# Kernel tuning notes

Measured on AMD Instinct MI355X. Metric: run time of the kernel, lower is better.

## Reference

```python
import jax, jax.numpy as jnp
import numpy as np

B_SZ, SEQ, D_IN, D_ST, D_OUT = 16, 8192, 128, 128, 128


def setup_inputs() -> dict:
    key = jax.random.key(0)
    ku, ka, kb, kc, kd = jax.random.split(key, 5)
    u = jax.random.normal(ku, (B_SZ, SEQ, D_IN), dtype=jnp.float32)
    # A scaled to spectral radius ~0.9 so the long recurrence stays stable
    A = jax.random.normal(ka, (D_ST, D_ST), dtype=jnp.float32) * (0.9 / np.sqrt(D_ST))
    B = jax.random.normal(kb, (D_ST, D_IN), dtype=jnp.float32) * (1.0 / np.sqrt(D_IN))
    C = jax.random.normal(kc, (D_OUT, D_ST), dtype=jnp.float32) * (1.0 / np.sqrt(D_ST))
    D = jax.random.normal(kd, (D_OUT, D_IN), dtype=jnp.float32) * (1.0 / np.sqrt(D_IN))
    return {"u": u, "A": A, "B": B, "C": C, "D": D}


def reference(u, A, B, C, D):
    # x_t = x_{t-1} A^T + u_t B^T ; y_t = x_t C^T + u_t D^T ; x_0 = 0
    batch = u.shape[0]
    state0 = jnp.zeros((batch, A.shape[0]), dtype=u.dtype)

    def step(state, u_t):  # state: [B, S_dim], u_t: [B, D_in]
        new_state = state @ A.T + u_t @ B.T
        y = new_state @ C.T + u_t @ D.T
        return new_state, y

    u_t_first = jnp.swapaxes(u, 0, 1)  # [SEQ, B, D_in]
    _, ys = jax.lax.scan(step, state0, u_t_first)
    return jnp.swapaxes(ys, 0, 1)  # [B, SEQ, D_out]
```

## Files before the change

kernel.cpp:

```cpp
#include <hip/hip_runtime.h>


#define SEQ 8192
#define BS  16
#define DD  128
#define CL  32
#define NC  256
#define GRP 16
#define NG  16

typedef __bf16 bf16t;
typedef __bf16 bf16x8 __attribute__((ext_vector_type(8)));
typedef __bf16 bf16x4 __attribute__((ext_vector_type(4)));
typedef float  f32x4  __attribute__((ext_vector_type(4)));

#define MFMA(a,b,c) __builtin_amdgcn_mfma_f32_16x16x32_bf16(a,b,c,0,0,0)

__device__ __forceinline__ int swz(int b, int j) { return j ^ ((b & 7) << 3); }

struct Frag { bf16x8 h[4]; bf16x8 l[4]; };

__device__ __forceinline__ void load_frag_T(const float* __restrict__ src, int lane, int w, Frag& f) {
    int n  = (w << 4) + (lane & 15);
    int kb = ((lane >> 4) & 3) << 3;
#pragma unroll
    for (int q = 0; q < 4; q++) {
        const float* p = src + n * DD + (q << 5) + kb;
#pragma unroll
        for (int e = 0; e < 8; e++) {
            float v = p[e];
            bf16t hh = (bf16t)v;
            f.h[q][e] = hh;
            f.l[q][e] = (bf16t)(v - (float)hh);
        }
    }
}

__device__ __forceinline__ void load_frag_N(const float* __restrict__ src, int lane, int w, Frag& f) {
    int n  = (w << 4) + (lane & 15);
    int kb = ((lane >> 4) & 3) << 3;
#pragma unroll
    for (int q = 0; q < 4; q++) {
#pragma unroll
        for (int e = 0; e < 8; e++) {
            float v = src[((q << 5) + kb + e) * DD + n];
            bf16t hh = (bf16t)v;
            f.h[q][e] = hh;
            f.l[q][e] = (bf16t)(v - (float)hh);
        }
    }
}

__device__ __forceinline__ bf16x8 afrag(const bf16t* __restrict__ X, int lane, int q) {
    int b  = lane & 15;
    int j0 = (q << 5) + (((lane >> 4) & 3) << 3);
    return *(const bf16x8*)(X + b * DD + swz(b, j0));
}

__device__ __forceinline__ void put_state(bf16t* __restrict__ H, bf16t* __restrict__ L,
                                          int lane, int w, f32x4 acc) {
    int n = (w << 4) + (lane & 15);
#pragma unroll
    for (int r = 0; r < 4; r++) {
        int b = (((lane >> 4) & 3) << 2) + r;
        float v = acc[r];
        bf16t hh = (bf16t)v;
        H[b * DD + swz(b, n)] = hh;
        L[b * DD + swz(b, n)] = (bf16t)(v - (float)hh);
    }
}

__device__ __forceinline__ void stage_rows(const float* __restrict__ src, long rs,
                                           bf16t* __restrict__ H, bf16t* __restrict__ L, int tid) {
    int b  = tid >> 5;
    int j0 = (tid & 31) << 2;
    float4 v = *(const float4*)(src + (long)b * rs + j0);
    float vv[4] = { v.x, v.y, v.z, v.w };
    bf16x4 h, l;
#pragma unroll
    for (int e = 0; e < 4; e++) {
        bf16t hh = (bf16t)vv[e];
        h[e] = hh;
        l[e] = (bf16t)(vv[e] - (float)hh);
    }
    *(bf16x4*)(H + b * DD + swz(b, j0)) = h;
    *(bf16x4*)(L + b * DD + swz(b, j0)) = l;
}

__device__ __forceinline__ f32x4 load_accfrag(const float* __restrict__ src, int lane, int w) {
    int n = (w << 4) + (lane & 15);
    f32x4 a;
#pragma unroll
    for (int r = 0; r < 4; r++) {
        int b = (((lane >> 4) & 3) << 2) + r;
        a[r] = src[b * DD + n];
    }
    return a;
}

__device__ __forceinline__ void store_accfrag(float* __restrict__ dst, int lane, int w,
                                              f32x4 a, long rs) {
    int n = (w << 4) + (lane & 15);
#pragma unroll
    for (int r = 0; r < 4; r++) {
        int b = (((lane >> 4) & 3) << 2) + r;
        dst[(long)b * rs + n] = a[r];
    }
}

__global__ __launch_bounds__(512) void k_chunk(const float* __restrict__ u,
                                               const float* __restrict__ A,
                                               const float* __restrict__ B,
                                               float* __restrict__ E,
                                               float* __restrict__ P) {
    __shared__ __align__(16) bf16t Xh[2][BS * DD], Xl[2][BS * DD];
    __shared__ __align__(16) bf16t Uh[2][BS * DD], Ul[2][BS * DD];
    int tid = threadIdx.x, lane = tid & 63, w = tid >> 6;
    bool ident = blockIdx.x >= NC;
    int g2 = blockIdx.x - NC;

    Frag fA, fB;
    load_frag_T(A, lane, w, fA);
    if (!ident) load_frag_T(B, lane, w, fB);

    for (int i = tid; i < BS * DD; i += 512) {
        int b = i >> 7, j = swz(b, i & 127);
        float v = (ident && j == g2 * 16 + b) ? 1.f : 0.f;
        Xh[0][i] = (bf16t)v;
        Xl[0][i] = (bf16t)0.f;
    }
    int c = blockIdx.x;
    const float* ubase = u + (long)c * CL * DD;
    int b_ = tid >> 5, j0_ = (tid & 31) << 2;
    if (!ident) stage_rows(ubase, (long)SEQ * DD, Uh[0], Ul[0], tid);
    __syncthreads();

    int p = 0;
    f32x4 acc = {0.f, 0.f, 0.f, 0.f};
    for (int i = 0; i < CL; i++) {
        float4 un = {0.f, 0.f, 0.f, 0.f};
        if (!ident && i + 1 < CL)
            un = *(const float4*)(ubase + (long)b_ * SEQ * DD + (i + 1) * DD + j0_);
        f32x4 ax = {0.f,0.f,0.f,0.f}, ax2 = {0.f,0.f,0.f,0.f};
#pragma unroll
        for (int q = 0; q < 4; q++) {
            bf16x8 xh = afrag(Xh[p], lane, q), xl = afrag(Xl[p], lane, q);
            ax  = MFMA(xh, fA.h[q], ax);
            ax2 = MFMA(xl, fA.h[q], ax2);
            ax  = MFMA(xh, fA.l[q], ax);
            if (!ident) {
                bf16x8 uh = afrag(Uh[i & 1], lane, q), ul = afrag(Ul[i & 1], lane, q);
                ax2 = MFMA(uh, fB.h[q], ax2);
                ax  = MFMA(ul, fB.h[q], ax);
                ax2 = MFMA(uh, fB.l[q], ax2);
            }
        }
        acc = ax + ax2;
        if (i + 1 < CL) {
            put_state(Xh[p ^ 1], Xl[p ^ 1], lane, w, acc);
            if (!ident) {
                float vv[4] = { un.x, un.y, un.z, un.w };
                bf16x4 h, l;
#pragma unroll
                for (int e = 0; e < 4; e++) {
                    bf16t hh = (bf16t)vv[e];
                    h[e] = hh;
                    l[e] = (bf16t)(vv[e] - (float)hh);
                }
                *(bf16x4*)(Uh[(i + 1) & 1] + b_ * DD + swz(b_, j0_)) = h;
                *(bf16x4*)(Ul[(i + 1) & 1] + b_ * DD + swz(b_, j0_)) = l;
            }
            __syncthreads();
            p ^= 1;
        }
    }
    if (!ident) store_accfrag(E + (long)c * BS * DD, lane, w, acc, DD);
    else        store_accfrag(P + (long)g2 * 16 * DD, lane, w, acc, DD);
}

__global__ __launch_bounds__(512) void k_group(const float* __restrict__ E,
                                               const float* __restrict__ P,
                                               float* __restrict__ E2,
                                               float* __restrict__ Pg) {
    __shared__ __align__(16) bf16t Xh[2][BS * DD], Xl[2][BS * DD];
    int tid = threadIdx.x, lane = tid & 63, w = tid >> 6;
    bool ident = blockIdx.x >= NG;
    int g2 = blockIdx.x - NG;
    Frag fP;
    load_frag_N(P, lane, w, fP);
    for (int i = tid; i < BS * DD; i += 512) {
        int b = i >> 7, j = swz(b, i & 127);
        float v = (ident && j == g2 * 16 + b) ? 1.f : 0.f;
        Xh[0][i] = (bf16t)v;
        Xl[0][i] = (bf16t)0.f;
    }
    __syncthreads();
    int p = 0, g = blockIdx.x;
    f32x4 acc = {0.f, 0.f, 0.f, 0.f};
    for (int r = 0; r < GRP; r++) {
        f32x4 a1 = {0.f,0.f,0.f,0.f}, a2 = {0.f,0.f,0.f,0.f};
        if (!ident) a1 = load_accfrag(E + (long)(g * GRP + r) * BS * DD, lane, w);
#pragma unroll
        for (int q = 0; q < 4; q++) {
            bf16x8 xh = afrag(Xh[p], lane, q), xl = afrag(Xl[p], lane, q);
            a1 = MFMA(xh, fP.h[q], a1);
            a2 = MFMA(xl, fP.h[q], a2);
            a1 = MFMA(xh, fP.l[q], a1);
        }
        acc = a1 + a2;
        if (r + 1 < GRP) {
            put_state(Xh[p ^ 1], Xl[p ^ 1], lane, w, acc);
            __syncthreads();
            p ^= 1;
        }
    }
    if (!ident) store_accfrag(E2 + (long)g * BS * DD, lane, w, acc, DD);
    else        store_accfrag(Pg + (long)g2 * 16 * DD, lane, w, acc, DD);
}

__global__ __launch_bounds__(512) void k_top(const float* __restrict__ E2,
                                             const float* __restrict__ Pg,
                                             float* __restrict__ S2) {
    __shared__ __align__(16) bf16t Xh[2][BS * DD], Xl[2][BS * DD];
    int tid = threadIdx.x, lane = tid & 63, w = tid >> 6;
    Frag fP;
    load_frag_N(Pg, lane, w, fP);
    for (int i = tid; i < BS * DD; i += 512) {
        Xh[0][i] = (bf16t)0.f;
        Xl[0][i] = (bf16t)0.f;
    }
    __syncthreads();
    int p = 0;
    f32x4 T = {0.f, 0.f, 0.f, 0.f};
    for (int g = 0; g < NG; g++) {
        store_accfrag(S2 + (long)g * BS * DD, lane, w, T, DD);
        f32x4 a1 = load_accfrag(E2 + (long)g * BS * DD, lane, w), a2 = {0.f,0.f,0.f,0.f};
#pragma unroll
        for (int q = 0; q < 4; q++) {
            bf16x8 xh = afrag(Xh[p], lane, q), xl = afrag(Xl[p], lane, q);
            a1 = MFMA(xh, fP.h[q], a1);
            a2 = MFMA(xl, fP.h[q], a2);
            a1 = MFMA(xh, fP.l[q], a1);
        }
        T = a1 + a2;
        if (g + 1 < NG) {
            put_state(Xh[p ^ 1], Xl[p ^ 1], lane, w, T);
            __syncthreads();
            p ^= 1;
        }
    }
}

__global__ __launch_bounds__(512) void k_fix(const float* __restrict__ E,
                                             const float* __restrict__ P,
                                             const float* __restrict__ S2,
                                             float* __restrict__ S) {
    __shared__ __align__(16) bf16t Xh[2][BS * DD], Xl[2][BS * DD];
    int tid = threadIdx.x, lane = tid & 63, w = tid >> 6;
    int g = blockIdx.x;
    Frag fP;
    load_frag_N(P, lane, w, fP);
    stage_rows(S2 + (long)g * BS * DD, DD, Xh[0], Xl[0], tid);
    f32x4 T = load_accfrag(S2 + (long)g * BS * DD, lane, w);
    __syncthreads();
    int p = 0;
    for (int r = 0; r < GRP; r++) {
        int c = g * GRP + r;
        store_accfrag(S + (long)c * BS * DD, lane, w, T, DD);
        if (r + 1 == GRP) break;
        f32x4 a1 = load_accfrag(E + (long)c * BS * DD, lane, w), a2 = {0.f,0.f,0.f,0.f};
#pragma unroll
        for (int q = 0; q < 4; q++) {
            bf16x8 xh = afrag(Xh[p], lane, q), xl = afrag(Xl[p], lane, q);
            a1 = MFMA(xh, fP.h[q], a1);
            a2 = MFMA(xl, fP.h[q], a2);
            a1 = MFMA(xh, fP.l[q], a1);
        }
        T = a1 + a2;
        put_state(Xh[p ^ 1], Xl[p ^ 1], lane, w, T);
        __syncthreads();
        p ^= 1;
    }
}

__global__ __launch_bounds__(512) void k_main(const float* __restrict__ u,
                                              const float* __restrict__ A,
                                              const float* __restrict__ B,
                                              const float* __restrict__ C,
                                              const float* __restrict__ D,
                                              const float* __restrict__ S,
                                              float* __restrict__ out) {
    __shared__ __align__(16) bf16t Xh[2][BS * DD], Xl[2][BS * DD];
    __shared__ __align__(16) bf16t Uh[2][BS * DD], Ul[2][BS * DD];
    int tid = threadIdx.x, lane = tid & 63, w = tid >> 6;
    Frag fA, fB, fC, fD;
    load_frag_T(A, lane, w, fA);
    load_frag_T(B, lane, w, fB);
    load_frag_T(C, lane, w, fC);
    load_frag_T(D, lane, w, fD);
    int c = blockIdx.x;
    const float* ubase = u + (long)c * CL * DD;
    int b_ = tid >> 5, j0_ = (tid & 31) << 2;
    stage_rows(S + (long)c * BS * DD, DD, Xh[0], Xl[0], tid);
    stage_rows(ubase, (long)SEQ * DD, Uh[0], Ul[0], tid);
    __syncthreads();
    int p = 0;
    for (int i = 0; i < CL; i++) {
        float4 un = {0.f, 0.f, 0.f, 0.f};
        if (i + 1 < CL)
            un = *(const float4*)(ubase + (long)b_ * SEQ * DD + (i + 1) * DD + j0_);
        f32x4 ax = {0.f,0.f,0.f,0.f}, ax2 = {0.f,0.f,0.f,0.f};
        f32x4 ay = {0.f,0.f,0.f,0.f}, ay2 = {0.f,0.f,0.f,0.f};
#pragma unroll
        for (int q = 0; q < 4; q++) {
            bf16x8 xh = afrag(Xh[p], lane, q), xl = afrag(Xl[p], lane, q);
            bf16x8 uh = afrag(Uh[i & 1], lane, q), ul = afrag(Ul[i & 1], lane, q);
            ax  = MFMA(xh, fA.h[q], ax);
            ax2 = MFMA(xl, fA.h[q], ax2);
            ax  = MFMA(xh, fA.l[q], ax);
            ax2 = MFMA(uh, fB.h[q], ax2);
            ax  = MFMA(ul, fB.h[q], ax);
            ax2 = MFMA(uh, fB.l[q], ax2);
            ay  = MFMA(uh, fD.h[q], ay);
            ay2 = MFMA(ul, fD.h[q], ay2);
            ay  = MFMA(uh, fD.l[q], ay);
        }
        f32x4 xnew = ax + ax2;
        put_state(Xh[p ^ 1], Xl[p ^ 1], lane, w, xnew);
        if (i + 1 < CL) {
            float vv[4] = { un.x, un.y, un.z, un.w };
            bf16x4 h, l;
#pragma unroll
            for (int e = 0; e < 4; e++) {
                bf16t hh = (bf16t)vv[e];
                h[e] = hh;
                l[e] = (bf16t)(vv[e] - (float)hh);
            }
            *(bf16x4*)(Uh[(i + 1) & 1] + b_ * DD + swz(b_, j0_)) = h;
            *(bf16x4*)(Ul[(i + 1) & 1] + b_ * DD + swz(b_, j0_)) = l;
        }
        __syncthreads();
#pragma unroll
        for (int q = 0; q < 4; q++) {
            bf16x8 nh = afrag(Xh[p ^ 1], lane, q), nl = afrag(Xl[p ^ 1], lane, q);
            ay  = MFMA(nh, fC.h[q], ay);
            ay2 = MFMA(nl, fC.h[q], ay2);
            ay  = MFMA(nh, fC.l[q], ay);
        }
        f32x4 y = ay + ay2;
        store_accfrag(out + ((long)c * CL + i) * DD, lane, w, y, (long)SEQ * DD);
        p ^= 1;
    }
}

extern "C" void kernel_launch(void* const* d_in, const int* in_sizes, int n_in,
                              void* d_out, int out_size, void* d_ws, size_t ws_size,
                              hipStream_t stream) {
    (void)in_sizes; (void)n_in; (void)out_size; (void)ws_size;
    const float* u = (const float*)d_in[0];
    const float* A = (const float*)d_in[1];
    const float* B = (const float*)d_in[2];
    const float* C = (const float*)d_in[3];
    const float* D = (const float*)d_in[4];
    float* out = (float*)d_out;
    float* ws  = (float*)d_ws;
    float* P  = ws;
    float* Pg = ws + 16384;
    float* E  = ws + 32768;
    float* E2 = ws + 32768 + 524288;
    float* S2 = E2 + 32768;
    float* S  = S2 + 32768;
    dim3 blk(512);
    k_chunk<<<NC + 8, blk, 0, stream>>>(u, A, B, E, P);
    k_group<<<NG + 8, blk, 0, stream>>>(E, P, E2, Pg);
    k_top  <<<1,      blk, 0, stream>>>(E2, Pg, S2);
    k_fix  <<<NG,     blk, 0, stream>>>(E, P, S2, S);
    k_main <<<NC,     blk, 0, stream>>>(u, A, B, C, D, S, out);
}
```

Baseline: 131.7 us.

## Advance recurrence two steps per iteration using precomputed A², AB, CA, CAA products

Precomputes A², AB, CA, CA+D-style combined matrices in two small prep kernels, then advances the state two timesteps per iteration in both the chunk and main kernels. This halves the number of serial dependency steps and barriers per chunk. Outputs are computed directly from the previous state and inputs, so the second C-multiply after the barrier goes away. Output matrices use only the high bf16 part (no split-precision correction), which risks lower accuracy. It also adds two prep launches and more register pressure, with launch bounds hinting two blocks per CU.

```diff
diff --git a/kernel.cpp b/kernel.cpp
--- a/kernel.cpp
+++ b/kernel.cpp
@@ -5,6 +5,7 @@
 #define BS  16
 #define DD  128
 #define CL  32
+#define PH  16
 #define NC  256
 #define GRP 16
 #define NG  16
@@ -18,7 +19,8 @@
 
 __device__ __forceinline__ int swz(int b, int j) { return j ^ ((b & 7) << 3); }
 
-struct Frag { bf16x8 h[4]; bf16x8 l[4]; };
+struct Frag  { bf16x8 h[4]; bf16x8 l[4]; };
+struct FragH { bf16x8 h[4]; };
 
 __device__ __forceinline__ void load_frag_T(const float* __restrict__ src, int lane, int w, Frag& f) {
     int n  = (w << 4) + (lane & 15);
@@ -33,6 +35,17 @@
             f.h[q][e] = hh;
             f.l[q][e] = (bf16t)(v - (float)hh);
         }
+    }
+}
+
+__device__ __forceinline__ void load_frag_T_h(const float* __restrict__ src, int lane, int w, FragH& f) {
+    int n  = (w << 4) + (lane & 15);
+    int kb = ((lane >> 4) & 3) << 3;
+#pragma unroll
+    for (int q = 0; q < 4; q++) {
+        const float* p = src + n * DD + (q << 5) + kb;
+#pragma unroll
+        for (int e = 0; e < 8; e++) f.h[q][e] = (bf16t)p[e];
     }
 }
 
@@ -87,6 +100,20 @@
     *(bf16x4*)(L + b * DD + swz(b, j0)) = l;
 }
 
+__device__ __forceinline__ void write_u(bf16t* __restrict__ H, bf16t* __restrict__ L,
+                                        int b_, int j0_, float4 v) {
+    float vv[4] = { v.x, v.y, v.z, v.w };
+    bf16x4 h, l;
+#pragma unroll
+    for (int e = 0; e < 4; e++) {
+        bf16t hh = (bf16t)vv[e];
+        h[e] = hh;
+        l[e] = (bf16t)(vv[e] - (float)hh);
+    }
+    *(bf16x4*)(H + b_ * DD + swz(b_, j0_)) = h;
+    *(bf16x4*)(L + b_ * DD + swz(b_, j0_)) = l;
+}
+
 __device__ __forceinline__ f32x4 load_accfrag(const float* __restrict__ src, int lane, int w) {
     int n = (w << 4) + (lane & 15);
     f32x4 a;
@@ -108,20 +135,51 @@
     }
 }
 
-__global__ __launch_bounds__(512) void k_chunk(const float* __restrict__ u,
-                                               const float* __restrict__ A,
+__global__ __launch_bounds__(128) void k_prep1(const float* __restrict__ A,
                                                const float* __restrict__ B,
-                                               float* __restrict__ E,
-                                               float* __restrict__ P) {
+                                               const float* __restrict__ C,
+                                               const float* __restrict__ D,
+                                               float* __restrict__ A2m, float* __restrict__ ABm,
+                                               float* __restrict__ Gm,  float* __restrict__ Hm) {
+    int sel = blockIdx.x >> 7, r = blockIdx.x & 127, j = threadIdx.x;
+    const float* L = (sel < 2) ? A : C;
+    const float* R = (sel == 0 || sel == 2) ? A : B;
+    float s = 0.f;
+#pragma unroll 8
+    for (int m = 0; m < 128; m++) s = fmaf(L[r * 128 + m], R[m * 128 + j], s);
+    if      (sel == 0) A2m[r * 128 + j] = s;
+    else if (sel == 1) ABm[r * 128 + j] = s;
+    else if (sel == 2) Gm[r * 128 + j]  = s;
+    else               Hm[r * 128 + j]  = s + D[r * 128 + j];
+}
+
+__global__ __launch_bounds__(128) void k_prep2(const float* __restrict__ A,
+                                               const float* __restrict__ B,
+                                               const float* __restrict__ Gm,
+                                               float* __restrict__ G2m, float* __restrict__ H2m) {
+    int sel = blockIdx.x >> 7, r = blockIdx.x & 127, j = threadIdx.x;
+    const float* R = sel ? B : A;
+    float s = 0.f;
+#pragma unroll 8
+    for (int m = 0; m < 128; m++) s = fmaf(Gm[r * 128 + m], R[m * 128 + j], s);
+    (sel ? H2m : G2m)[r * 128 + j] = s;
+}
+
+__global__ __launch_bounds__(512, 2) void k_chunk(const float* __restrict__ u,
+                                                  const float* __restrict__ A2m,
+                                                  const float* __restrict__ ABm,
+                                                  const float* __restrict__ Bm,
+                                                  float* __restrict__ E,
+                                                  float* __restrict__ P) {
     __shared__ __align__(16) bf16t Xh[2][BS * DD], Xl[2][BS * DD];
-    __shared__ __align__(16) bf16t Uh[2][BS * DD], Ul[2][BS * DD];
+    __shared__ __align__(16) bf16t Uh[2][2][BS * DD], Ul[2][2][BS * DD];
     int tid = threadIdx.x, lane = tid & 63, w = tid >> 6;
     bool ident = blockIdx.x >= NC;
     int g2 = blockIdx.x - NC;
 
-    Frag fA, fB;
-    load_frag_T(A, lane, w, fA);
-    if (!ident) load_frag_T(B, lane, w, fB);
+    Frag fA2, fAB, fB;
+    load_frag_T(A2m, lane, w, fA2);
+    if (!ident) { load_frag_T(ABm, lane, w, fAB); load_frag_T(Bm, lane, w, fB); }
 
     for (int i = tid; i < BS * DD; i += 512) {
         int b = i >> 7, j = swz(b, i & 127);
@@ -132,43 +190,46 @@
     int c = blockIdx.x;
     const float* ubase = u + (long)c * CL * DD;
     int b_ = tid >> 5, j0_ = (tid & 31) << 2;
-    if (!ident) stage_rows(ubase, (long)SEQ * DD, Uh[0], Ul[0], tid);
+    if (!ident) {
+        stage_rows(ubase,      (long)SEQ * DD, Uh[0][0], Ul[0][0], tid);
+        stage_rows(ubase + DD, (long)SEQ * DD, Uh[0][1], Ul[0][1], tid);
+    }
     __syncthreads();
 
     int p = 0;
     f32x4 acc = {0.f, 0.f, 0.f, 0.f};
-    for (int i = 0; i < CL; i++) {
-        float4 un = {0.f, 0.f, 0.f, 0.f};
-        if (!ident && i + 1 < CL)
-            un = *(const float4*)(ubase + (long)b_ * SEQ * DD + (i + 1) * DD + j0_);
-        f32x4 ax = {0.f,0.f,0.f,0.f}, ax2 = {0.f,0.f,0.f,0.f};
+    for (int j = 0; j < PH; j++) {
+        int jb = j & 1;
+        float4 un1 = {0,0,0,0}, un2 = {0,0,0,0};
+        if (!ident && j + 1 < PH) {
+            const float* nb = ubase + (long)b_ * SEQ * DD + (2 * j + 2) * DD + j0_;
+            un1 = *(const float4*)(nb);
+            un2 = *(const float4*)(nb + DD);
+        }
+        f32x4 ax = {0,0,0,0}, ax2 = {0,0,0,0}, ax3 = {0,0,0,0};
 #pragma unroll
         for (int q = 0; q < 4; q++) {
             bf16x8 xh = afrag(Xh[p], lane, q), xl = afrag(Xl[p], lane, q);
-            ax  = MFMA(xh, fA.h[q], ax);
-            ax2 = MFMA(xl, fA.h[q], ax2);
-            ax  = MFMA(xh, fA.l[q], ax);
+            ax  = MFMA(xh, fA2.h[q], ax);
+            ax2 = MFMA(xl, fA2.h[q], ax2);
+            ax3 = MFMA(xh, fA2.l[q], ax3);
             if (!ident) {
-                bf16x8 uh = afrag(Uh[i & 1], lane, q), ul = afrag(Ul[i & 1], lane, q);
-                ax2 = MFMA(uh, fB.h[q], ax2);
-                ax  = MFMA(ul, fB.h[q], ax);
-                ax2 = MFMA(uh, fB.l[q], ax2);
+                bf16x8 u1h = afrag(Uh[jb][0], lane, q), u1l = afrag(Ul[jb][0], lane, q);
+                bf16x8 u2h = afrag(Uh[jb][1], lane, q), u2l = afrag(Ul[jb][1], lane, q);
+                ax  = MFMA(u1h, fAB.h[q], ax);
+                ax2 = MFMA(u1l, fAB.h[q], ax2);
+                ax3 = MFMA(u1h, fAB.l[q], ax3);
+                ax  = MFMA(u2h, fB.h[q], ax);
+                ax2 = MFMA(u2l, fB.h[q], ax2);
+                ax3 = MFMA(u2h, fB.l[q], ax3);
             }
         }
-        acc = ax + ax2;
-        if (i + 1 < CL) {
+        acc = ax + ax2 + ax3;
+        if (j + 1 < PH) {
             put_state(Xh[p ^ 1], Xl[p ^ 1], lane, w, acc);
             if (!ident) {
-                float vv[4] = { un.x, un.y, un.z, un.w };
-                bf16x4 h, l;
-#pragma unroll
-                for (int e = 0; e < 4; e++) {
-                    bf16t hh = (bf16t)vv[e];
-                    h[e] = hh;
-                    l[e] = (bf16t)(vv[e] - (float)hh);
-                }
-                *(bf16x4*)(Uh[(i + 1) & 1] + b_ * DD + swz(b_, j0_)) = h;
-                *(bf16x4*)(Ul[(i + 1) & 1] + b_ * DD + swz(b_, j0_)) = l;
+                write_u(Uh[jb ^ 1][0], Ul[jb ^ 1][0], b_, j0_, un1);
+                write_u(Uh[jb ^ 1][1], Ul[jb ^ 1][1], b_, j0_, un2);
             }
             __syncthreads();
             p ^= 1;
@@ -283,73 +344,82 @@
     }
 }
 
-__global__ __launch_bounds__(512) void k_main(const float* __restrict__ u,
-                                              const float* __restrict__ A,
-                                              const float* __restrict__ B,
-                                              const float* __restrict__ C,
-                                              const float* __restrict__ D,
-                                              const float* __restrict__ S,
-                                              float* __restrict__ out) {
+__global__ __launch_bounds__(512, 2) void k_main(const float* __restrict__ u,
+                                                 const float* __restrict__ A2m,
+                                                 const float* __restrict__ ABm,
+                                                 const float* __restrict__ Bm,
+                                                 const float* __restrict__ Gm,
+                                                 const float* __restrict__ Hm,
+                                                 const float* __restrict__ G2m,
+                                                 const float* __restrict__ H2m,
+                                                 const float* __restrict__ S,
+                                                 float* __restrict__ out) {
     __shared__ __align__(16) bf16t Xh[2][BS * DD], Xl[2][BS * DD];
-    __shared__ __align__(16) bf16t Uh[2][BS * DD], Ul[2][BS * DD];
+    __shared__ __align__(16) bf16t Uh[2][2][BS * DD], Ul[2][2][BS * DD];
     int tid = threadIdx.x, lane = tid & 63, w = tid >> 6;
-    Frag fA, fB, fC, fD;
-    load_frag_T(A, lane, w, fA);
-    load_frag_T(B, lane, w, fB);
-    load_frag_T(C, lane, w, fC);
-    load_frag_T(D, lane, w, fD);
+    Frag fA2, fAB, fB;
+    FragH fG, fH, fG2, fH2;
+    load_frag_T(A2m, lane, w, fA2);
+    load_frag_T(ABm, lane, w, fAB);
+    load_frag_T(Bm,  lane, w, fB);
+    load_frag_T_h(Gm,  lane, w, fG);
+    load_frag_T_h(Hm,  lane, w, fH);
+    load_frag_T_h(G2m, lane, w, fG2);
+    load_frag_T_h(H2m, lane, w, fH2);
     int c = blockIdx.x;
     const float* ubase = u + (long)c * CL * DD;
     int b_ = tid >> 5, j0_ = (tid & 31) << 2;
     stage_rows(S + (long)c * BS * DD, DD, Xh[0], Xl[0], tid);
-    stage_rows(ubase, (long)SEQ * DD, Uh[0], Ul[0], tid);
+    stage_rows(ubase,      (long)SEQ * DD, Uh[0][0], Ul[0][0], tid);
+    stage_rows(ubase + DD, (long)SEQ * DD, Uh[0][1], Ul[0][1], tid);
     __syncthreads();
     int p = 0;
-    for (int i = 0; i < CL; i++) {
-        float4 un = {0.f, 0.f, 0.f, 0.f};
-        if (i + 1 < CL)
-            un = *(const float4*)(ubase + (long)b_ * SEQ * DD + (i + 1) * DD + j0_);
-        f32x4 ax = {0.f,0.f,0.f,0.f}, ax2 = {0.f,0.f,0.f,0.f};
-        f32x4 ay = {0.f,0.f,0.f,0.f}, ay2 = {0.f,0.f,0.f,0.f};
+    for (int j = 0; j < PH; j++) {
+        int jb = j & 1;
+        float4 un1 = {0,0,0,0}, un2 = {0,0,0,0};
+        if (j + 1 < PH) {
+            const float* nb = ubase + (long)b_ * SEQ * DD + (2 * j + 2) * DD + j0_;
+            un1 = *(const float4*)(nb);
+            un2 = *(const float4*)(nb + DD);
+        }
+        f32x4 ax = {0,0,0,0}, ax2 = {0,0,0,0}, ax3 = {0,0,0,0};
+        f32x4 ay1 = {0,0,0,0}, ay1b = {0,0,0,0};
+        f32x4 ay2 = {0,0,0,0}, ay2b = {0,0,0,0}, ay2c = {0,0,0,0};
 #pragma unroll
         for (int q = 0; q < 4; q++) {
-            bf16x8 xh = afrag(Xh[p], lane, q), xl = afrag(Xl[p], lane, q);
-            bf16x8 uh = afrag(Uh[i & 1], lane, q), ul = afrag(Ul[i & 1], lane, q);
-            ax  = MFMA(xh, fA.h[q], ax);
-            ax2 = MFMA(xl, fA.h[q], ax2);
-            ax  = MFMA(xh, fA.l[q], ax);
-            ax2 = MFMA(uh, fB.h[q], ax2);
-            ax  = MFMA(ul, fB.h[q], ax);
-            ax2 = MFMA(uh, fB.l[q], ax2);
-            ay  = MFMA(uh, fD.h[q], ay);
-            ay2 = MFMA(ul, fD.h[q], ay2);
-            ay  = MFMA(uh, fD.l[q], ay);
-        }
-        f32x4 xnew = ax + ax2;
-        put_state(Xh[p ^ 1], Xl[p ^ 1], lane, w, xnew);
-        if (i + 1 < CL) {
-            float vv[4] = { un.x, un.y, un.z, un.w };
-            bf16x4 h, l;
-#pragma unroll
-            for (int e = 0; e < 4; e++) {
-                bf16t hh = (bf16t)vv[e];
-                h[e] = hh;
-                l[e] = (bf16t)(vv[e] - (float)hh);
-            }
-            *(bf16x4*)(Uh[(i + 1) & 1] + b_ * DD + swz(b_, j0_)) = h;
-            *(bf16x4*)(Ul[(i + 1) & 1] + b_ * DD + swz(b_, j0_)) = l;
-        }
-        __syncthreads();
-#pragma unroll
-        for (int q = 0; q < 4; q++) {
-            bf16x8 nh = afrag(Xh[p ^ 1], lane, q), nl = afrag(Xl[p ^ 1], lane, q);
-            ay  = MFMA(nh, fC.h[q], ay);
-            ay2 = MFMA(nl, fC.h[q], ay2);
-            ay  = MFMA(nh, fC.l[q], ay);
-        }
-        f32x4 y = ay + ay2;
-        store_accfrag(out + ((long)c * CL + i) * DD, lane, w, y, (long)SEQ * DD);
-        p ^= 1;
+            bf16x8 xh  = afrag(Xh[p], lane, q),      xl  = afrag(Xl[p], lane, q);
+            bf16x8 u1h = afrag(Uh[jb][0], lane, q),  u1l = afrag(Ul[jb][0], lane, q);
+            bf16x8 u2h = afrag(Uh[jb][1], lane, q),  u2l = afrag(Ul[jb][1], lane, q);
+            ax  = MFMA(xh,  fA2.h[q], ax);
+            ax2 = MFMA(xl,  fA2.h[q], ax2);
+            ax3 = MFMA(xh,  fA2.l[q], ax3);
+            ax  = MFMA(u1h, fAB.h[q], ax);
+            ax2 = MFMA(u1l, fAB.h[q], ax2);
+            ax3 = MFMA(u1h, fAB.l[q], ax3);
+            ax  = MFMA(u2h, fB.h[q],  ax);
+            ax2 = MFMA(u2l, fB.h[q],  ax2);
+            ax3 = MFMA(u2h, fB.l[q],  ax3);
+            ay1  = MFMA(xh,  fG.h[q],  ay1);
+            ay1b = MFMA(u1h, fH.h[q],  ay1b);
+            ay2  = MFMA(xh,  fG2.h[q], ay2);
+            ay2b = MFMA(u1h, fH2.h[q], ay2b);
+            ay2c = MFMA(u2h, fH.h[q],  ay2c);
+        }
+        f32x4 xnew = ax + ax2 + ax3;
+        if (j + 1 < PH) {
+            put_state(Xh[p ^ 1], Xl[p ^ 1], lane, w, xnew);
+            write_u(Uh[jb ^ 1][0], Ul[jb ^ 1][0], b_, j0_, un1);
+            write_u(Uh[jb ^ 1][1], Ul[jb ^ 1][1], b_, j0_, un2);
+        }
+        f32x4 y1 = ay1 + ay1b;
+        f32x4 y2 = ay2 + ay2b + ay2c;
+        long t0 = (long)c * CL + 2 * j;
+        store_accfrag(out + t0 * DD,       lane, w, y1, (long)SEQ * DD);
+        store_accfrag(out + (t0 + 1) * DD, lane, w, y2, (long)SEQ * DD);
+        if (j + 1 < PH) {
+            __syncthreads();
+            p ^= 1;
+        }
     }
 }
 
@@ -364,16 +434,24 @@
     const float* D = (const float*)d_in[4];
     float* out = (float*)d_out;
     float* ws  = (float*)d_ws;
-    float* P  = ws;
-    float* Pg = ws + 16384;
-    float* E  = ws + 32768;
-    float* E2 = ws + 32768 + 524288;
-    float* S2 = E2 + 32768;
-    float* S  = S2 + 32768;
+    float* P   = ws;
+    float* Pg  = P   + 16384;
+    float* A2m = Pg  + 16384;
+    float* ABm = A2m + 16384;
+    float* Gm  = ABm + 16384;
+    float* Hm  = Gm  + 16384;
+    float* G2m = Hm  + 16384;
+    float* H2m = G2m + 16384;
+    float* E   = H2m + 16384;
+    float* E2  = E   + 524288;
+    float* S2  = E2  + 32768;
+    float* S   = S2  + 32768;
     dim3 blk(512);
-    k_chunk<<<NC + 8, blk, 0, stream>>>(u, A, B, E, P);
+    k_prep1<<<512, 128, 0, stream>>>(A, B, C, D, A2m, ABm, Gm, Hm);
+    k_prep2<<<256, 128, 0, stream>>>(A, B, Gm, G2m, H2m);
+    k_chunk<<<NC + 8, blk, 0, stream>>>(u, A2m, ABm, B, E, P);
     k_group<<<NG + 8, blk, 0, stream>>>(E, P, E2, Pg);
     k_top  <<<1,      blk, 0, stream>>>(E2, Pg, S2);
     k_fix  <<<NG,     blk, 0, stream>>>(E, P, S2, S);
-    k_main <<<NC,     blk, 0, stream>>>(u, A, B, C, D, S, out);
-}
+    k_main <<<NC,     blk, 0, stream>>>(u, A2m, ABm, B, Gm, Hm, G2m, H2m, S, out);
+}
```

Result: slower. 134.4 us (+2.0%).
